# Kernel optimization log

Measured on AMD Instinct MI355X. Metric: run time of the kernel, lower is better.

Reference implementation:

```python
import jax, jax.numpy as jnp
import numpy as np

N = 100000      # num_nodes
E = 600000      # edges per relation
R = 3           # num_relations
F_IN = 128
F_OUT = 64


def setup_inputs() -> dict:
    key = jax.random.key(0)
    k0, k1, k2, k3 = jax.random.split(key, 4)
    x = jax.random.normal(k0, (N, F_IN), dtype=jnp.float32)
    edge_indices = jax.random.randint(k1, (R, 2, E), 0, N, dtype=jnp.int32)
    # torch.randperm per relation -> fixed permutations as int inputs
    perms = jnp.stack([jax.random.permutation(jax.random.fold_in(k2, r), N).astype(jnp.int32)
                       for r in range(R)])
    # GCNConv glorot weight + zero bias, one per relation
    Ws = jax.random.normal(k3, (R, F_IN, F_OUT), dtype=jnp.float32) * (1.0 / np.sqrt(F_IN))
    bs = jnp.zeros((R, F_OUT), dtype=jnp.float32)
    return {"x": x, "edge_indices": edge_indices, "perms": perms, "Ws": Ws, "bs": bs}


def gcn_conv(h, src, dst, W, b, n):
    """PyG GCNConv: add self-loops, sym-normalize, linear, scatter-sum, bias."""
    loops = jnp.arange(n, dtype=src.dtype)
    s = jnp.concatenate([src, loops])
    d = jnp.concatenate([dst, loops])
    deg = jax.ops.segment_sum(jnp.ones_like(s, dtype=h.dtype), d, num_segments=n)
    dinv = jnp.where(deg > 0, jax.lax.rsqrt(deg), 0.0)
    norm = dinv[s] * dinv[d]                      # [E+n]
    hw = h @ W                                    # [n, F_OUT]
    out = jax.ops.segment_sum(hw[s] * norm[:, None], d, num_segments=n)
    return out + b


def reference(x, edge_indices, perms, Ws, bs):
    # Eval mode: F.dropout(p=0.5, training=False) is identity.
    n = x.shape[0]
    pos_hs, neg_hs, summaries = [], [], []
    for r in range(R):
        src, dst = edge_indices[r, 0], edge_indices[r, 1]
        pos_h = jax.nn.relu(gcn_conv(x, src, dst, Ws[r], bs[r], n))
        neg_h = jax.nn.relu(gcn_conv(x[perms[r]], src, dst, Ws[r], bs[r], n))
        pos_hs.append(pos_h)
        neg_hs.append(neg_h)
        summaries.append(pos_h.mean(axis=0, keepdims=True))
    return (jnp.stack(pos_hs), jnp.stack(neg_hs), jnp.stack(summaries))
```

## Files before the change

### kernel.cpp

```cpp
#include <hip/hip_runtime.h>

#define F_IN 128
#define F_OUT 64
#define CAP 32

typedef float f32x2 __attribute__((ext_vector_type(2)));
typedef float f32x4 __attribute__((ext_vector_type(4)));
typedef short bf16x8 __attribute__((ext_vector_type(8)));

__device__ __forceinline__ unsigned short f2bf(float f) {
    unsigned int u = __float_as_uint(f);
    u += 0x7fff + ((u >> 16) & 1);
    return (unsigned short)(u >> 16);
}
__device__ __forceinline__ float bf2f(unsigned short s) {
    return __uint_as_float((unsigned int)s << 16);
}

__global__ __launch_bounds__(256) void prep_kernel(const int* __restrict__ ei,
                                                   const int* __restrict__ perm,
                                                   const float* __restrict__ W,
                                                   int* __restrict__ deg,
                                                   int2* __restrict__ csr,
                                                   unsigned short* __restrict__ wt_hi,
                                                   unsigned short* __restrict__ wt_lo,
                                                   int N, int E, int R, int degB) {
    int b = blockIdx.x;
    if (b < degB) {
        int idx = b * 256 + threadIdx.x;
        if (idx < R * E) {
            int r = idx / E, e = idx - r * E;
            const int* base = ei + (size_t)r * 2 * E;
            int s = base[e], d = base[E + e];
            int pos = atomicAdd(&deg[(size_t)r * N + d], 1) & (CAP - 1);
            int ps = perm[(size_t)r * N + s];
            int2 sp; sp.x = s; sp.y = ps;
            csr[((size_t)r * N + d) * CAP + pos] = sp;
        }
    } else {
        int idx = (b - degB) * 256 + threadIdx.x;
        if (idx < R * 64 * 128) {
            int k = idx & 127, c = (idx >> 7) & 63, r = idx >> 13;
            float v = W[((size_t)r * F_IN + k) * F_OUT + c];
            unsigned short h = f2bf(v);
            wt_hi[idx] = h;
            wt_lo[idx] = f2bf(v - bf2f(h));
        }
    }
}

__global__ __launch_bounds__(256) void gemm_xw(const float* __restrict__ x,
                                               const unsigned short* __restrict__ wt_hi,
                                               const unsigned short* __restrict__ wt_lo,
                                               unsigned short* __restrict__ hw,
                                               int N, int R) {
    constexpr int KP = 136;
    __shared__ __align__(16) unsigned short xs_hi[64 * KP];
    __shared__ __align__(16) unsigned short xs_lo[64 * KP];

    int row0 = blockIdx.x * 64;
    int tid = threadIdx.x;
    {
        int rr = tid >> 2, q = tid & 3;
        int grow = row0 + rr; if (grow >= N) grow = N - 1;
        const float* xr = x + (size_t)grow * F_IN + q * 32;
        unsigned short* dh = &xs_hi[rr * KP + q * 32];
        unsigned short* dl = &xs_lo[rr * KP + q * 32];
        #pragma unroll
        for (int c = 0; c < 32; c += 4) {
            float4 v = *(const float4*)(xr + c);
            unsigned short h0 = f2bf(v.x), h1 = f2bf(v.y),
                           h2 = f2bf(v.z), h3 = f2bf(v.w);
            ushort4 hv; hv.x = h0; hv.y = h1; hv.z = h2; hv.w = h3;
            *(ushort4*)(dh + c) = hv;
            ushort4 lv;
            lv.x = f2bf(v.x - bf2f(h0)); lv.y = f2bf(v.y - bf2f(h1));
            lv.z = f2bf(v.z - bf2f(h2)); lv.w = f2bf(v.w - bf2f(h3));
            *(ushort4*)(dl + c) = lv;
        }
    }
    __syncthreads();

    int wv = tid >> 6, lane = tid & 63;
    int l15 = lane & 15, lhi = lane >> 4;
    int nbase = wv * 16;
    for (int r = 0; r < R; ++r) {
        f32x4 acc[4];
        #pragma unroll
        for (int ct = 0; ct < 4; ++ct) acc[ct] = (f32x4){0.f, 0.f, 0.f, 0.f};
        const unsigned short* wh = wt_hi + (size_t)r * 64 * 128;
        const unsigned short* wl = wt_lo + (size_t)r * 64 * 128;
        #pragma unroll
        for (int kc = 0; kc < 4; ++kc) {
            int kb = kc * 32 + lhi * 8;
            int ro = (nbase + l15) * KP + kb;
            bf16x8 bh = *(const bf16x8*)&xs_hi[ro];
            bf16x8 bl = *(const bf16x8*)&xs_lo[ro];
            bf16x8 ah[4], al[4];
            #pragma unroll
            for (int ct = 0; ct < 4; ++ct) {
                int wo = (ct * 16 + l15) * 128 + kb;
                ah[ct] = *(const bf16x8*)(wh + wo);
                al[ct] = *(const bf16x8*)(wl + wo);
            }
            #pragma unroll
            for (int ct = 0; ct < 4; ++ct) {
                acc[ct] = __builtin_amdgcn_mfma_f32_16x16x32_bf16(ah[ct], bh, acc[ct], 0, 0, 0);
                acc[ct] = __builtin_amdgcn_mfma_f32_16x16x32_bf16(ah[ct], bl, acc[ct], 0, 0, 0);
                acc[ct] = __builtin_amdgcn_mfma_f32_16x16x32_bf16(al[ct], bh, acc[ct], 0, 0, 0);
            }
        }
        size_t rb = (size_t)r * N;
        int xrow = row0 + nbase + l15;
        if (xrow < N) {
            #pragma unroll
            for (int ct = 0; ct < 4; ++ct) {
                f32x4 a = acc[ct];
                ushort4 v;
                v.x = f2bf(a.x); v.y = f2bf(a.y);
                v.z = f2bf(a.z); v.w = f2bf(a.w);
                int cb = ct * 16 + lhi * 4;
                *(ushort4*)(hw + (rb + xrow) * 64 + cb) = v;
            }
        }
    }
}

__global__ __launch_bounds__(256) void gather_kernel(const int2* __restrict__ csr,
                                                     const int* __restrict__ deg,
                                                     const unsigned short* __restrict__ hw,
                                                     const int* __restrict__ perm,
                                                     const float* __restrict__ bs,
                                                     float* __restrict__ out_pos,
                                                     float* __restrict__ out_neg,
                                                     float* __restrict__ partial,
                                                     int N, int perRel) {
    int bid = blockIdx.x;
    int r = bid / perRel, ib = bid - r * perRel;
    int lane = threadIdx.x & 63, wv = threadIdx.x >> 6;
    int i = __builtin_amdgcn_readfirstlane(ib * 4 + wv);
    int half = lane >> 5;
    int c0 = (lane & 31) * 2;
    __shared__ float ls[4][64];
    float p0 = 0.f, p1 = 0.f;
    if (i < N) {
        const unsigned short* hwr = hw + (size_t)r * N * 64;
        const int* dgr = deg + (size_t)r * N;
        const int2* cs = csr + (size_t)r * N * CAP;
        int d = __builtin_amdgcn_readfirstlane(dgr[i]);
        float dinv_d = rsqrtf((float)(d + 1));
        float w = dinv_d * dinv_d;
        int pi = __builtin_amdgcn_readfirstlane(perm[(size_t)r * N + i]);
        int selfrow = half ? pi : i;
        unsigned int sv = *(const unsigned int*)(hwr + (size_t)selfrow * 64 + c0);
        float acc0 = bf2f((unsigned short)sv) * w;
        float acc1 = bf2f((unsigned short)(sv >> 16)) * w;
        size_t rowb = (size_t)i * CAP;
        int last = d - 1;
        for (int j = 0; j < d; j += 8) {
            int src8[8]; float nm8[8];
            #pragma unroll
            for (int k = 0; k < 8; ++k) {
                int idx = j + k;
                int ic = idx < last ? idx : last;
                int2 e = cs[rowb + ic];
                int sdeg = dgr[e.x];
                float nrm = rsqrtf((float)(sdeg + 1)) * dinv_d;
                src8[k] = half ? e.y : e.x;
                nm8[k] = (idx < d) ? nrm : 0.f;
            }
            #pragma unroll
            for (int k = 0; k < 8; ++k) {
                unsigned int v = *(const unsigned int*)(hwr + (size_t)src8[k] * 64 + c0);
                acc0 += bf2f((unsigned short)v) * nm8[k];
                acc1 += bf2f((unsigned short)(v >> 16)) * nm8[k];
            }
        }
        float2 bv = *(const float2*)(bs + r * F_OUT + c0);
        float q0 = acc0 + bv.x; q0 = q0 > 0.f ? q0 : 0.f;
        float q1 = acc1 + bv.y; q1 = q1 > 0.f ? q1 : 0.f;
        size_t off = (size_t)r * N * F_OUT + (size_t)i * F_OUT + c0;
        float* dst = (lane < 32) ? (out_pos + off) : (out_neg + off);
        f32x2 o; o.x = q0; o.y = q1;
        __builtin_nontemporal_store(o, (f32x2*)dst);
        if (lane < 32) { p0 = q0; p1 = q1; }
    }
    if (lane < 32) { ls[wv][c0] = p0; ls[wv][c0 + 1] = p1; }
    __syncthreads();
    if (wv == 0) {
        float t = ls[0][lane] + ls[1][lane] + ls[2][lane] + ls[3][lane];
        atomicAdd(&partial[((size_t)r * 256 + (ib & 255)) * F_OUT + lane], t);
    }
}

__global__ __launch_bounds__(256) void summary_reduce(const float* __restrict__ partial,
                                                      float* __restrict__ summary,
                                                      float inv_n) {
    int r = blockIdx.x;
    int lane = threadIdx.x & 63, wv = threadIdx.x >> 6;
    __shared__ float ls[256];
    float s = 0.f;
    for (int c = wv; c < 256; c += 4)
        s += partial[((size_t)r * 256 + c) * F_OUT + lane];
    ls[threadIdx.x] = s;
    __syncthreads();
    if (wv == 0)
        summary[r * F_OUT + lane] =
            (ls[lane] + ls[64 + lane] + ls[128 + lane] + ls[192 + lane]) * inv_n;
}

extern "C" void kernel_launch(void* const* d_in, const int* in_sizes, int n_in,
                              void* d_out, int out_size, void* d_ws, size_t ws_size,
                              hipStream_t stream) {
    const float* x    = (const float*)d_in[0];
    const int*   ei   = (const int*)d_in[1];
    const int*   perm = (const int*)d_in[2];
    const float* Ws   = (const float*)d_in[3];
    const float* bs   = (const float*)d_in[4];

    const int N = in_sizes[0] / F_IN;
    const int R = in_sizes[4] / F_OUT;
    const int E = in_sizes[1] / (2 * R);

    float* out_pos = (float*)d_out;
    float* out_neg = out_pos + (size_t)R * N * F_OUT;
    float* summary = out_neg + (size_t)R * N * F_OUT;

    char* ws = (char*)d_ws;
    size_t off = 0;
    auto alloc = [&](size_t bytes) { void* p = ws + off;
        off += (bytes + 255) & ~(size_t)255; return p; };
    int*   deg      = (int*)  alloc((size_t)R * N * 4);
    float* partial  = (float*)alloc((size_t)R * 256 * F_OUT * 4);
    int2*  csr      = (int2*) alloc((size_t)R * N * CAP * 8);
    unsigned short* hw = (unsigned short*)alloc((size_t)R * N * 64 * 2);
    unsigned short* wt_hi = (unsigned short*)alloc((size_t)R * 64 * 128 * 2);
    unsigned short* wt_lo = (unsigned short*)alloc((size_t)R * 64 * 128 * 2);

    const int degB = (R * E + 255) / 256;
    const int wB   = (R * 64 * 128 + 255) / 256;
    const int gemmB = (N + 63) / 64;
    const int perRel = (N + 3) / 4;

    size_t zbytes = (size_t)((char*)csr - (char*)deg);
    hipMemsetAsync(deg, 0, zbytes, stream);

    prep_kernel<<<degB + wB, 256, 0, stream>>>(ei, perm, Ws, deg, csr,
                                               wt_hi, wt_lo, N, E, R, degB);
    gemm_xw<<<gemmB, 256, 0, stream>>>(x, wt_hi, wt_lo, hw, N, R);
    gather_kernel<<<perRel * R, 256, 0, stream>>>(csr, deg, hw, perm, bs,
                                                  out_pos, out_neg, partial,
                                                  N, perRel);
    summary_reduce<<<R, 256, 0, stream>>>(partial, summary, 1.0f / (float)N);
}
```

Before: 623.3 us.

## Precompute permuted GEMM rows and source normalization into an interleaved pos/neg buffer

The GEMM now also computes the negative-branch rows from perm-gathered x and scales every row by the source degree's rsqrt. Both halves are written into one 128-wide bf16 row per node, so the gather reads a single contiguous row per edge. It also no longer loads a source degree or perm per edge. The CSR shrinks to plain source indices, at the cost of doubling GEMM work and adding a perm gather of x.

Result: slower. 675.3 us (+8.3%).

```diff
diff --git a/kernel.cpp b/kernel.cpp
--- a/kernel.cpp
+++ b/kernel.cpp
@@ -18,10 +18,9 @@
 }
 
 __global__ __launch_bounds__(256) void prep_kernel(const int* __restrict__ ei,
-                                                   const int* __restrict__ perm,
                                                    const float* __restrict__ W,
                                                    int* __restrict__ deg,
-                                                   int2* __restrict__ csr,
+                                                   int* __restrict__ csr,
                                                    unsigned short* __restrict__ wt_hi,
                                                    unsigned short* __restrict__ wt_lo,
                                                    int N, int E, int R, int degB) {
@@ -33,9 +32,7 @@
             const int* base = ei + (size_t)r * 2 * E;
             int s = base[e], d = base[E + e];
             int pos = atomicAdd(&deg[(size_t)r * N + d], 1) & (CAP - 1);
-            int ps = perm[(size_t)r * N + s];
-            int2 sp; sp.x = s; sp.y = ps;
-            csr[((size_t)r * N + d) * CAP + pos] = sp;
+            csr[((size_t)r * N + d) * CAP + pos] = s;
         }
     } else {
         int idx = (b - degB) * 256 + threadIdx.x;
@@ -52,7 +49,9 @@
 __global__ __launch_bounds__(256) void gemm_xw(const float* __restrict__ x,
                                                const unsigned short* __restrict__ wt_hi,
                                                const unsigned short* __restrict__ wt_lo,
-                                               unsigned short* __restrict__ hw,
+                                               const int* __restrict__ perm,
+                                               const int* __restrict__ deg,
+                                               unsigned short* __restrict__ combined,
                                                int N, int R) {
     constexpr int KP = 136;
     __shared__ __align__(16) unsigned short xs_hi[64 * KP];
@@ -60,10 +59,14 @@
 
     int row0 = blockIdx.x * 64;
     int tid = threadIdx.x;
-    {
-        int rr = tid >> 2, q = tid & 3;
-        int grow = row0 + rr; if (grow >= N) grow = N - 1;
-        const float* xr = x + (size_t)grow * F_IN + q * 32;
+    int rr = tid >> 2, q = tid & 3;
+    int sgrow = row0 + rr; if (sgrow >= N) sgrow = N - 1;
+    int wv = tid >> 6, lane = tid & 63;
+    int l15 = lane & 15, lhi = lane >> 4;
+    int nbase = wv * 16;
+    int xrow = row0 + nbase + l15;
+
+    auto stage = [&](const float* xr) {
         unsigned short* dh = &xs_hi[rr * KP + q * 32];
         unsigned short* dl = &xs_lo[rr * KP + q * 32];
         #pragma unroll
@@ -78,14 +81,8 @@
             lv.z = f2bf(v.z - bf2f(h2)); lv.w = f2bf(v.w - bf2f(h3));
             *(ushort4*)(dl + c) = lv;
         }
-    }
-    __syncthreads();
-
-    int wv = tid >> 6, lane = tid & 63;
-    int l15 = lane & 15, lhi = lane >> 4;
-    int nbase = wv * 16;
-    for (int r = 0; r < R; ++r) {
-        f32x4 acc[4];
+    };
+    auto compute = [&](int r, f32x4* acc) {
         #pragma unroll
         for (int ct = 0; ct < 4; ++ct) acc[ct] = (f32x4){0.f, 0.f, 0.f, 0.f};
         const unsigned short* wh = wt_hi + (size_t)r * 64 * 128;
@@ -96,40 +93,53 @@
             int ro = (nbase + l15) * KP + kb;
             bf16x8 bh = *(const bf16x8*)&xs_hi[ro];
             bf16x8 bl = *(const bf16x8*)&xs_lo[ro];
-            bf16x8 ah[4], al[4];
             #pragma unroll
             for (int ct = 0; ct < 4; ++ct) {
                 int wo = (ct * 16 + l15) * 128 + kb;
-                ah[ct] = *(const bf16x8*)(wh + wo);
-                al[ct] = *(const bf16x8*)(wl + wo);
+                bf16x8 ah = *(const bf16x8*)(wh + wo);
+                bf16x8 al = *(const bf16x8*)(wl + wo);
+                acc[ct] = __builtin_amdgcn_mfma_f32_16x16x32_bf16(ah, bh, acc[ct], 0, 0, 0);
+                acc[ct] = __builtin_amdgcn_mfma_f32_16x16x32_bf16(ah, bl, acc[ct], 0, 0, 0);
+                acc[ct] = __builtin_amdgcn_mfma_f32_16x16x32_bf16(al, bh, acc[ct], 0, 0, 0);
             }
-            #pragma unroll
-            for (int ct = 0; ct < 4; ++ct) {
-                acc[ct] = __builtin_amdgcn_mfma_f32_16x16x32_bf16(ah[ct], bh, acc[ct], 0, 0, 0);
-                acc[ct] = __builtin_amdgcn_mfma_f32_16x16x32_bf16(ah[ct], bl, acc[ct], 0, 0, 0);
-                acc[ct] = __builtin_amdgcn_mfma_f32_16x16x32_bf16(al[ct], bh, acc[ct], 0, 0, 0);
-            }
-        }
+        }
+    };
+    auto store_half = [&](int r, const f32x4* acc, int halfoff) {
+        if (xrow >= N) return;
+        float dv = rsqrtf((float)(deg[(size_t)r * N + xrow] + 1));
         size_t rb = (size_t)r * N;
-        int xrow = row0 + nbase + l15;
-        if (xrow < N) {
-            #pragma unroll
-            for (int ct = 0; ct < 4; ++ct) {
-                f32x4 a = acc[ct];
-                ushort4 v;
-                v.x = f2bf(a.x); v.y = f2bf(a.y);
-                v.z = f2bf(a.z); v.w = f2bf(a.w);
-                int cb = ct * 16 + lhi * 4;
-                *(ushort4*)(hw + (rb + xrow) * 64 + cb) = v;
-            }
-        }
-    }
-}
-
-__global__ __launch_bounds__(256) void gather_kernel(const int2* __restrict__ csr,
+        #pragma unroll
+        for (int ct = 0; ct < 4; ++ct) {
+            f32x4 a = acc[ct];
+            ushort4 v;
+            v.x = f2bf(a.x * dv); v.y = f2bf(a.y * dv);
+            v.z = f2bf(a.z * dv); v.w = f2bf(a.w * dv);
+            int cb = ct * 16 + lhi * 4;
+            *(ushort4*)(combined + (rb + xrow) * 128 + halfoff + cb) = v;
+        }
+    };
+
+    stage(x + (size_t)sgrow * F_IN + q * 32);
+    __syncthreads();
+    for (int r = 0; r < R; ++r) {
+        f32x4 acc[4];
+        compute(r, acc);
+        store_half(r, acc, 0);
+    }
+    for (int r = 0; r < R; ++r) {
+        __syncthreads();
+        int prow = perm[(size_t)r * N + sgrow];
+        stage(x + (size_t)prow * F_IN + q * 32);
+        __syncthreads();
+        f32x4 acc[4];
+        compute(r, acc);
+        store_half(r, acc, 64);
+    }
+}
+
+__global__ __launch_bounds__(256) void gather_kernel(const int* __restrict__ csr,
                                                      const int* __restrict__ deg,
-                                                     const unsigned short* __restrict__ hw,
-                                                     const int* __restrict__ perm,
+                                                     const unsigned short* __restrict__ combined,
                                                      const float* __restrict__ bs,
                                                      float* __restrict__ out_pos,
                                                      float* __restrict__ out_neg,
@@ -139,46 +149,39 @@
     int r = bid / perRel, ib = bid - r * perRel;
     int lane = threadIdx.x & 63, wv = threadIdx.x >> 6;
     int i = __builtin_amdgcn_readfirstlane(ib * 4 + wv);
-    int half = lane >> 5;
     int c0 = (lane & 31) * 2;
     __shared__ float ls[4][64];
     float p0 = 0.f, p1 = 0.f;
     if (i < N) {
-        const unsigned short* hwr = hw + (size_t)r * N * 64;
-        const int* dgr = deg + (size_t)r * N;
-        const int2* cs = csr + (size_t)r * N * CAP;
-        int d = __builtin_amdgcn_readfirstlane(dgr[i]);
-        float dinv_d = rsqrtf((float)(d + 1));
-        float w = dinv_d * dinv_d;
-        int pi = __builtin_amdgcn_readfirstlane(perm[(size_t)r * N + i]);
-        int selfrow = half ? pi : i;
-        unsigned int sv = *(const unsigned int*)(hwr + (size_t)selfrow * 64 + c0);
-        float acc0 = bf2f((unsigned short)sv) * w;
-        float acc1 = bf2f((unsigned short)(sv >> 16)) * w;
+        const unsigned short* cw = combined + (size_t)r * N * 128;
+        const int* cs = csr + (size_t)r * N * CAP;
+        int d = __builtin_amdgcn_readfirstlane(deg[(size_t)r * N + i]);
+        int dd = min(d, CAP);
+        float dv = rsqrtf((float)(d + 1));
+        unsigned int sv = *(const unsigned int*)(cw + (size_t)i * 128 + 2 * lane);
+        float acc0 = bf2f((unsigned short)sv);
+        float acc1 = bf2f((unsigned short)(sv >> 16));
         size_t rowb = (size_t)i * CAP;
-        int last = d - 1;
-        for (int j = 0; j < d; j += 8) {
-            int src8[8]; float nm8[8];
+        int last = dd - 1;
+        for (int j = 0; j < dd; j += 8) {
+            int s8[8]; float m8[8];
             #pragma unroll
             for (int k = 0; k < 8; ++k) {
                 int idx = j + k;
                 int ic = idx < last ? idx : last;
-                int2 e = cs[rowb + ic];
-                int sdeg = dgr[e.x];
-                float nrm = rsqrtf((float)(sdeg + 1)) * dinv_d;
-                src8[k] = half ? e.y : e.x;
-                nm8[k] = (idx < d) ? nrm : 0.f;
+                s8[k] = cs[rowb + ic];
+                m8[k] = (idx < dd) ? 1.f : 0.f;
             }
             #pragma unroll
             for (int k = 0; k < 8; ++k) {
-                unsigned int v = *(const unsigned int*)(hwr + (size_t)src8[k] * 64 + c0);
-                acc0 += bf2f((unsigned short)v) * nm8[k];
-                acc1 += bf2f((unsigned short)(v >> 16)) * nm8[k];
+                unsigned int v = *(const unsigned int*)(cw + (size_t)s8[k] * 128 + 2 * lane);
+                acc0 += bf2f((unsigned short)v) * m8[k];
+                acc1 += bf2f((unsigned short)(v >> 16)) * m8[k];
             }
         }
         float2 bv = *(const float2*)(bs + r * F_OUT + c0);
-        float q0 = acc0 + bv.x; q0 = q0 > 0.f ? q0 : 0.f;
-        float q1 = acc1 + bv.y; q1 = q1 > 0.f ? q1 : 0.f;
+        float q0 = acc0 * dv + bv.x; q0 = q0 > 0.f ? q0 : 0.f;
+        float q1 = acc1 * dv + bv.y; q1 = q1 > 0.f ? q1 : 0.f;
         size_t off = (size_t)r * N * F_OUT + (size_t)i * F_OUT + c0;
         float* dst = (lane < 32) ? (out_pos + off) : (out_neg + off);
         f32x2 o; o.x = q0; o.y = q1;
@@ -232,8 +235,8 @@
         off += (bytes + 255) & ~(size_t)255; return p; };
     int*   deg      = (int*)  alloc((size_t)R * N * 4);
     float* partial  = (float*)alloc((size_t)R * 256 * F_OUT * 4);
-    int2*  csr      = (int2*) alloc((size_t)R * N * CAP * 8);
-    unsigned short* hw = (unsigned short*)alloc((size_t)R * N * 64 * 2);
+    int*   csr      = (int*)  alloc((size_t)R * N * CAP * 4);
+    unsigned short* combined = (unsigned short*)alloc((size_t)R * N * 128 * 2);
     unsigned short* wt_hi = (unsigned short*)alloc((size_t)R * 64 * 128 * 2);
     unsigned short* wt_lo = (unsigned short*)alloc((size_t)R * 64 * 128 * 2);
 
@@ -245,10 +248,10 @@
     size_t zbytes = (size_t)((char*)csr - (char*)deg);
     hipMemsetAsync(deg, 0, zbytes, stream);
 
-    prep_kernel<<<degB + wB, 256, 0, stream>>>(ei, perm, Ws, deg, csr,
+    prep_kernel<<<degB + wB, 256, 0, stream>>>(ei, Ws, deg, csr,
                                                wt_hi, wt_lo, N, E, R, degB);
-    gemm_xw<<<gemmB, 256, 0, stream>>>(x, wt_hi, wt_lo, hw, N, R);
-    gather_kernel<<<perRel * R, 256, 0, stream>>>(csr, deg, hw, perm, bs,
+    gemm_xw<<<gemmB, 256, 0, stream>>>(x, wt_hi, wt_lo, perm, deg, combined, N, R);
+    gather_kernel<<<perRel * R, 256, 0, stream>>>(csr, deg, combined, bs,
                                                   out_pos, out_neg, partial,
                                                   N, perRel);
     summary_reduce<<<R, 256, 0, stream>>>(partial, summary, 1.0f / (float)N);
```
